# Kernel tuning notes

Measured on AMD Instinct MI355X. Metric: run time of the kernel, lower is better.

## Reference

```python
import jax, jax.numpy as jnp
import numpy as np

NUM_HEADS = 16


def setup_inputs() -> dict:
    key = jax.random.key(0)
    k1, k2, k3, k4 = jax.random.split(key, 4)
    B, N, C = 4, 1024, 1024
    x = jax.random.normal(k1, (B, N, C), dtype=jnp.float32)
    mask = jnp.ones((B, N), dtype=jnp.float32)  # 1 = visible token
    # 0.02 init scale keeps logits in a sane range (avoids saturated softmax)
    W_qkv = jax.random.normal(k2, (C, 3 * C), dtype=jnp.float32) * 0.02
    W_proj = jax.random.normal(k3, (C, C), dtype=jnp.float32) * 0.02
    b_proj = jax.random.normal(k4, (C,), dtype=jnp.float32) * 0.02
    return {"x": x, "mask": mask, "W_qkv": W_qkv, "W_proj": W_proj, "b_proj": b_proj}


def reference(x, mask, W_qkv, W_proj, b_proj):
    B, N, C = x.shape
    H = NUM_HEADS
    D = C // H
    scale = D ** -0.5
    qkv = (x @ W_qkv).reshape(B, N, 3, H, D)
    q, k, v = qkv[:, :, 0], qkv[:, :, 1], qkv[:, :, 2]  # each [B, N, H, D]
    attn = jnp.einsum("bnhd,bmhd->bhnm", q, k) * scale  # [B, H, N, N]
    attn = attn + (1.0 - mask)[:, None, None, :] * -5.0  # additive mask penalty
    attn = jax.nn.softmax(attn, axis=-1)
    out = jnp.einsum("bhnm,bmhd->bnhd", attn, v).reshape(B, N, C)
    return out @ W_proj + b_proj
```

## Files before the change

### kernel.cpp

```cpp
#include <hip/hip_runtime.h>

typedef __attribute__((ext_vector_type(8))) short bf16x8;
typedef __attribute__((ext_vector_type(4))) float f32x4;
typedef __attribute__((ext_vector_type(16))) float f32x16;
typedef __attribute__((ext_vector_type(4))) float fl4;
typedef __attribute__((ext_vector_type(8))) unsigned short u16x8;
typedef __attribute__((ext_vector_type(4))) unsigned short u16x4;
typedef __attribute__((ext_vector_type(2))) int i32x2;
typedef __attribute__((ext_vector_type(4))) int i32x4;

#define MFMA16(A,B,C) __builtin_amdgcn_mfma_f32_16x16x32_bf16((A),(B),(C),0,0,0)
#define MFMA32(A,B,C) __builtin_amdgcn_mfma_f32_32x32x16_bf16((A),(B),(C),0,0,0)

#if __has_builtin(__builtin_amdgcn_exp2f)
#define EXP2R(x) __builtin_amdgcn_exp2f(x)
#else
#define EXP2R(x) exp2f(x)
#endif

__device__ __forceinline__ unsigned short f2bf_bits(float x) {
  union { float f; unsigned u; } v; v.f = x;
  unsigned r = v.u + 0x7fffu + ((v.u >> 16) & 1u);
  return (unsigned short)(r >> 16);
}

__device__ __forceinline__ void gload_lds16(const void* g, void* l) {
  __builtin_amdgcn_global_load_lds((const __attribute__((address_space(1))) void*)g,
                                   (__attribute__((address_space(3))) void*)l, 16, 0, 0);
}

__device__ __forceinline__ int cvtpk_bf16(float a, float b) {
  int r; asm("v_cvt_pk_bf16_f32 %0, %1, %2" : "=v"(r) : "v"(a), "v"(b)); return r;
}

__device__ __forceinline__ void plswap(int& a, int& b) {
#if __has_builtin(__builtin_amdgcn_permlane32_swap)
  i32x2 r = __builtin_amdgcn_permlane32_swap(a, b, false, false);
  a = r[0]; b = r[1];
#else
  asm volatile("s_nop 1\n\tv_permlane32_swap_b32 %0, %1" : "+v"(a), "+v"(b));
#endif
}

__global__ __launch_bounds__(256) void k_prep(const float* __restrict__ x,
                                              unsigned short* __restrict__ xb,
                                              const float* __restrict__ wqkv,
                                              unsigned short* __restrict__ dqkv,
                                              const float* __restrict__ wproj,
                                              unsigned short* __restrict__ dproj) {
  __shared__ float tile[64][65];
  const int bid = blockIdx.x;
  const int t = threadIdx.x;
  if (bid < 2048) {
    int i = (bid * 256 + t) * 8;
    fl4 a = *(const fl4*)(x + i);
    fl4 b = *(const fl4*)(x + i + 4);
    u16x8 o;
    o[0] = f2bf_bits(a[0]); o[1] = f2bf_bits(a[1]); o[2] = f2bf_bits(a[2]); o[3] = f2bf_bits(a[3]);
    o[4] = f2bf_bits(b[0]); o[5] = f2bf_bits(b[1]); o[6] = f2bf_bits(b[2]); o[7] = f2bf_bits(b[3]);
    *(u16x8*)(xb + i) = o;
    return;
  }
  const int idx = bid - 2048;
  const int bx = idx & 63, by = idx >> 6;
  const float* src; unsigned short* dst; int NCOL, nt;
  if (bx < 48) { src = wqkv; dst = dqkv; NCOL = 3072; nt = bx * 64; }
  else         { src = wproj; dst = dproj; NCOL = 1024; nt = (bx - 48) * 64; }
  const float sc = (bx < 16) ? 0.18033688f : 1.0f;
  const int kt = by * 64;
  {
    int r = t >> 2, c0 = (t & 3) * 16;
    const float* s = src + (size_t)(kt + r) * NCOL + nt + c0;
    #pragma unroll
    for (int j = 0; j < 4; ++j) {
      fl4 v = *(const fl4*)(s + j * 4);
      tile[r][c0 + j * 4 + 0] = v[0]; tile[r][c0 + j * 4 + 1] = v[1];
      tile[r][c0 + j * 4 + 2] = v[2]; tile[r][c0 + j * 4 + 3] = v[3];
    }
  }
  __syncthreads();
  {
    int n = t >> 2, kc = (t & 3) * 16;
    unsigned short* d = dst + (size_t)(nt + n) * 1024 + kt + kc;
    u16x8 o0, o1;
    #pragma unroll
    for (int j = 0; j < 8; ++j) o0[j] = f2bf_bits(tile[kc + j][n] * sc);
    #pragma unroll
    for (int j = 0; j < 8; ++j) o1[j] = f2bf_bits(tile[kc + 8 + j][n] * sc);
    *(u16x8*)d = o0;
    *(u16x8*)(d + 8) = o1;
  }
}

template <int MODE>
__global__ __launch_bounds__(256) void k_gemm(const unsigned short* __restrict__ A,
                                              const unsigned short* __restrict__ Bt,
                                              unsigned short* __restrict__ qp,
                                              unsigned short* __restrict__ kp,
                                              unsigned short* __restrict__ vtp,
                                              const float* __restrict__ bias,
                                              float* __restrict__ outp) {
  __shared__ __align__(16) char lds[49152];
  const int tid = threadIdx.x, lane = tid & 63, w = tid >> 6;
  const int wm = w >> 1, wn = w & 1;
  const int m0 = blockIdx.y * 128, n0 = blockIdx.x * 128;
  const char* Ab = (const char*)A + (size_t)m0 * 2048;
  const char* Bb = (const char*)Bt + (size_t)n0 * 2048;

  int goff[2];
  #pragma unroll
  for (int i = 0; i < 2; ++i) {
    int c = i * 256 + tid;
    int lr = c >> 3, s = c & 7, p = s >> 2, kc = (s & 3) ^ (lr & 3);
    goff[i] = (((lr << 1) | p) * 2048) + (kc << 4);
  }

  int afo[4], bfo[4];
  #pragma unroll
  for (int mi = 0; mi < 4; ++mi) {
    int tr = wm * 64 + mi * 16 + (lane & 15), kc = lane >> 4;
    afo[mi] = (tr >> 1) * 128 + (tr & 1) * 64 + (((kc ^ ((tr >> 1) & 3))) << 4);
  }
  #pragma unroll
  for (int ni = 0; ni < 4; ++ni) {
    int tr = wn * 64 + ni * 16 + (lane & 15), kc = lane >> 4;
    bfo[ni] = (tr >> 1) * 128 + (tr & 1) * 64 + (((kc ^ ((tr >> 1) & 3))) << 4);
  }

  f32x4 acc[4][4];
  #pragma unroll
  for (int mi = 0; mi < 4; ++mi)
    #pragma unroll
    for (int ni = 0; ni < 4; ++ni) acc[mi][ni] = f32x4{0.f, 0.f, 0.f, 0.f};

#define GSTAGE(BUF, T)                                                         \
  do {                                                                         \
    char* dA = lds + (BUF) * 16384 + tid * 16;                                 \
    char* dB = dA + 8192;                                                      \
    gload_lds16(Ab + goff[0] + (T) * 64, dA);                                  \
    gload_lds16(Ab + goff[1] + (T) * 64, dA + 4096);                           \
    gload_lds16(Bb + goff[0] + (T) * 64, dB);                                  \
    gload_lds16(Bb + goff[1] + (T) * 64, dB + 4096);                           \
  } while (0)

#define GCOMP(BUF)                                                             \
  do {                                                                         \
    const char* LA = lds + (BUF) * 16384;                                      \
    const char* LB = LA + 8192;                                                \
    bf16x8 af[4], bfv[4];                                                      \
    _Pragma("unroll") for (int mi = 0; mi < 4; ++mi)                           \
      af[mi] = *(const bf16x8*)(LA + afo[mi]);                                 \
    _Pragma("unroll") for (int ni = 0; ni < 4; ++ni)                           \
      bfv[ni] = *(const bf16x8*)(LB + bfo[ni]);                                \
    _Pragma("unroll") for (int mi = 0; mi < 4; ++mi)                           \
      _Pragma("unroll") for (int ni = 0; ni < 4; ++ni)                         \
        acc[mi][ni] = MFMA16(af[mi], bfv[ni], acc[mi][ni]);                    \
  } while (0)

  GSTAGE(0, 0);
  GSTAGE(1, 1);
  {
    int bc = 0, bs = 2;
    for (int j = 0; j < 31; ++j) {
      asm volatile("s_waitcnt vmcnt(4)" ::: "memory");
      __builtin_amdgcn_s_barrier();
      if (j < 30) GSTAGE(bs, j + 2);
      GCOMP(bc);
      bc = (bc == 2) ? 0 : bc + 1;
      bs = (bs == 2) ? 0 : bs + 1;
    }
    asm volatile("s_waitcnt vmcnt(0)" ::: "memory");
    __builtin_amdgcn_s_barrier();
    GCOMP(1);
  }
#undef GCOMP
#undef GSTAGE

  if (MODE == 0) {
    #pragma unroll
    for (int mi = 0; mi < 4; ++mi) {
      int row0 = m0 + wm * 64 + mi * 16 + ((lane >> 4) << 2);
      int bb = row0 >> 10, nn0 = row0 & 1023;
      #pragma unroll
      for (int ni = 0; ni < 4; ++ni) {
        int col = n0 + wn * 64 + ni * 16 + (lane & 15);
        int tt = col >> 10, rem = col & 1023, h = rem >> 6, d = rem & 63;
        f32x4 a = acc[mi][ni];
        if (tt == 2) {
          u16x4 pv;
          pv[0] = f2bf_bits(a[0]); pv[1] = f2bf_bits(a[1]);
          pv[2] = f2bf_bits(a[2]); pv[3] = f2bf_bits(a[3]);
          *(u16x4*)(vtp + (((size_t)(bb * 16 + h) * 64 + d) << 10) + nn0) = pv;
        } else {
          unsigned short* dst = (tt == 0) ? qp : kp;
          size_t base = ((size_t)(bb * 16 + h)) << 16;
          #pragma unroll
          for (int r = 0; r < 4; ++r)
            dst[base + (size_t)(nn0 + r) * 64 + d] = f2bf_bits(a[r]);
        }
      }
    }
  } else {
    #pragma unroll
    for (int mi = 0; mi < 4; ++mi) {
      int row0 = m0 + wm * 64 + mi * 16 + ((lane >> 4) << 2);
      #pragma unroll
      for (int ni = 0; ni < 4; ++ni) {
        int col = n0 + wn * 64 + ni * 16 + (lane & 15);
        float bv = bias[col];
        f32x4 a = acc[mi][ni];
        #pragma unroll
        for (int r = 0; r < 4; ++r)
          outp[(size_t)(row0 + r) * 1024 + col] = a[r] + bv;
      }
    }
  }
}

__global__ __launch_bounds__(512, 4) void k_attn(const unsigned short* __restrict__ qp,
                                                 const unsigned short* __restrict__ kp,
                                                 const unsigned short* __restrict__ vtp,
                                                 const float* __restrict__ mask,
                                                 unsigned short* __restrict__ aop) {
  __shared__ __align__(16) char lds[49152];
  const int tid = threadIdx.x, lane = tid & 63, w = tid >> 6;
  const int hi = lane >> 5, lq = lane & 31;
  const int pair = w >> 2, qsub = w & 3;
  const int g = blockIdx.x;
  const int bh = (g & 7) * 8 + ((g >> 6) & 7);
  const int qc = (g >> 3) & 7;
  const int b = bh >> 4, h = bh & 15;
  const char* kb = (const char*)(kp + ((size_t)bh << 16));
  const char* vb = (const char*)(vtp + ((size_t)bh << 16));
  const unsigned short* qh = qp + ((size_t)bh << 16);
  const float* mrow = mask + b * 1024 + pair * 512;
  const int q0 = qc * 128 + qsub * 32;

  const int kpk = tid >> 8, krow = (tid >> 3) & 31, kslot = tid & 7;
  const char* gK = kb + (size_t)kpk * 65536 + (size_t)krow * 128
                   + ((kslot ^ (krow & 7)) * 16);
  const int vpk = tid >> 8, vrow = (tid >> 2) & 63, vslot = tid & 3;
  const char* gV = vb + (size_t)vpk * 1024 + (size_t)vrow * 2048
                   + ((vslot ^ ((vrow >> 1) & 3)) * 16);
  char* const dK = lds + tid * 16;
  char* const dV = lds + 8192 + tid * 16;

  int kfo[4], vfo[4];
  #pragma unroll
  for (int dc = 0; dc < 4; ++dc)
    kfo[dc] = lq * 128 + (((dc << 1) | hi) ^ (lq & 7)) * 16;
  #pragma unroll
  for (int ks = 0; ks < 2; ++ks)
    #pragma unroll
    for (int nb = 0; nb < 2; ++nb) {
      int row = nb * 32 + lq;
      vfo[ks * 2 + nb] = row * 64 + (((ks << 1) | hi) ^ ((row >> 1) & 3)) * 16;
    }

  int bws[16];
  #pragma unroll
  for (int t2 = 0; t2 < 16; ++t2) {
    float mv = mrow[t2 * 32 + lq];
    bws[t2] = (hi == 0) ? (int)f2bf_bits(fmaf(mv, 7.2134752f, -12.9842554f)) : 0;
  }

  bf16x8 qB[4];
  #pragma unroll
  for (int dc = 0; dc < 4; ++dc)
    qB[dc] = *(const bf16x8*)(qh + (q0 + lq) * 64 + dc * 16 + hi * 8);

  i32x4 onesw = {hi == 0 ? 0x3F80 : 0, 0, 0, 0};
  const bf16x8 onesB = __builtin_bit_cast(bf16x8, onesw);

  f32x16 Z16;
  #pragma unroll
  for (int i = 0; i < 16; ++i) Z16[i] = 0.f;

  f32x16 O0, O1;
  #pragma unroll
  for (int i = 0; i < 16; ++i) { O0[i] = 0.f; O1[i] = 0.f; }
  float lsum = 0.f;

#define STAGE(BUF, T)                                                          \
  do {                                                                         \
    gload_lds16(gK + (T) * 4096, dK + (BUF) * 16384);                          \
    gload_lds16(gV + (T) * 64,   dV + (BUF) * 16384);                          \
  } while (0)

#define VMCNT(N) asm volatile("s_waitcnt vmcnt(" #N ")" ::: "memory")

#define STEP(BUF, T, N)                                                        \
  do {                                                                         \
    VMCNT(N);                                                                  \
    __builtin_amdgcn_s_barrier();                                              \
    if ((T) + 2 <= 15) STAGE(((T) + 2) % 3, (T) + 2);                          \
    const char* K = lds + (BUF) * 16384 + pair * 4096;                         \
    const char* V = lds + (BUF) * 16384 + 8192 + pair * 4096;                  \
    f32x16 acc;                                                                \
    {                                                                          \
      i32x4 bwv = {bws[T], 0, 0, 0};                                           \
      acc = MFMA32(__builtin_bit_cast(bf16x8, bwv), onesB, Z16);               \
    }                                                                          \
    __builtin_amdgcn_s_setprio(1);                                             \
    _Pragma("unroll") for (int dc = 0; dc < 4; ++dc) {                         \
      bf16x8 kf = *(const bf16x8*)(K + kfo[dc]);                               \
      acc = MFMA32(kf, qB[dc], acc);                                           \
    }                                                                          \
    __builtin_amdgcn_s_setprio(0);                                             \
    float p[16];                                                               \
    _Pragma("unroll") for (int r = 0; r < 16; ++r) {                           \
      p[r] = EXP2R(acc[r]);                                                    \
      lsum += p[r];                                                            \
    }                                                                          \
    int X0 = cvtpk_bf16(p[0], p[1]),   X1 = cvtpk_bf16(p[2], p[3]);            \
    int Y0 = cvtpk_bf16(p[4], p[5]),   Y1 = cvtpk_bf16(p[6], p[7]);            \
    int Z0 = cvtpk_bf16(p[8], p[9]),   Z1 = cvtpk_bf16(p[10], p[11]);          \
    int W0 = cvtpk_bf16(p[12], p[13]), W1 = cvtpk_bf16(p[14], p[15]);          \
    plswap(X0, Y0); plswap(X1, Y1);                                            \
    plswap(Z0, W0); plswap(Z1, W1);                                            \
    i32x4 pa0v = {X0, X1, Y0, Y1};                                             \
    i32x4 pa1v = {Z0, Z1, W0, W1};                                             \
    const bf16x8 PA0 = __builtin_bit_cast(bf16x8, pa0v);                       \
    const bf16x8 PA1 = __builtin_bit_cast(bf16x8, pa1v);                       \
    bf16x8 va0 = *(const bf16x8*)(V + vfo[0]);                                 \
    bf16x8 va1 = *(const bf16x8*)(V + vfo[1]);                                 \
    bf16x8 vb0 = *(const bf16x8*)(V + vfo[2]);                                 \
    bf16x8 vb1 = *(const bf16x8*)(V + vfo[3]);                                 \
    __builtin_amdgcn_s_setprio(1);                                             \
    O0 = MFMA32(PA0, va0, O0);                                                 \
    O1 = MFMA32(PA0, va1, O1);                                                 \
    O0 = MFMA32(PA1, vb0, O0);                                                 \
    O1 = MFMA32(PA1, vb1, O1);                                                 \
    __builtin_amdgcn_s_setprio(0);                                             \
  } while (0)

  STAGE(0, 0);
  STAGE(1, 1);
  STEP(0, 0, 2);  STEP(1, 1, 2);  STEP(2, 2, 2);  STEP(0, 3, 2);
  STEP(1, 4, 2);  STEP(2, 5, 2);  STEP(0, 6, 2);  STEP(1, 7, 2);
  STEP(2, 8, 2);  STEP(0, 9, 2);  STEP(1, 10, 2); STEP(2, 11, 2);
  STEP(0, 12, 2); STEP(1, 13, 2); STEP(2, 14, 2); STEP(0, 15, 0);
#undef STEP
#undef VMCNT
#undef STAGE

  __syncthreads();
  float tot = lsum + __shfl_xor(lsum, 32);
  float* fx = (float*)lds;
  if (pair == 1) {
    int base = qsub * 64 * 34 + lane * 34;
    #pragma unroll
    for (int r = 0; r < 16; ++r) { fx[base + r] = O0[r]; fx[base + 16 + r] = O1[r]; }
    fx[base + 32] = tot;
  }
  __syncthreads();
  if (pair == 0) {
    int base = qsub * 64 * 34 + lane * 34;
    float invT = 1.0f / (tot + fx[base + 32]);
    #pragma unroll
    for (int r = 0; r < 16; ++r) {
      int qr = (r & 3) + 8 * (r >> 2) + 4 * hi;
      float iv = __shfl(invT, qr);
      float o0 = (O0[r] + fx[base + r]) * iv;
      float o1 = (O1[r] + fx[base + 16 + r]) * iv;
      size_t ob = (size_t)(b * 1024 + q0 + qr) * 1024 + h * 64 + lq;
      aop[ob] = f2bf_bits(o0);
      aop[ob + 32] = f2bf_bits(o1);
    }
  }
}

extern "C" void kernel_launch(void* const* d_in, const int* in_sizes, int n_in,
                              void* d_out, int out_size, void* d_ws, size_t ws_size,
                              hipStream_t stream) {
  const float* x     = (const float*)d_in[0];
  const float* mask  = (const float*)d_in[1];
  const float* wqkv  = (const float*)d_in[2];
  const float* wproj = (const float*)d_in[3];
  const float* bproj = (const float*)d_in[4];
  float* out = (float*)d_out;

  char* ws = (char*)d_ws;
  unsigned short* xb     = (unsigned short*)(ws);
  unsigned short* wqkvt  = (unsigned short*)(ws + 8388608);
  unsigned short* wprojt = (unsigned short*)(ws + 14680064);
  unsigned short* qbuf   = (unsigned short*)(ws + 16777216);
  unsigned short* kbuf   = (unsigned short*)(ws + 25165824);
  unsigned short* vtbuf  = (unsigned short*)(ws + 33554432);
  unsigned short* aobuf  = (unsigned short*)(ws + 41943040);

  k_prep<<<dim3(3072), dim3(256), 0, stream>>>(x, xb, wqkv, wqkvt, wproj, wprojt);
  k_gemm<0><<<dim3(24, 32), dim3(256), 0, stream>>>(xb, wqkvt, qbuf, kbuf, vtbuf, nullptr, nullptr);
  k_attn<<<dim3(512), dim3(512), 0, stream>>>(qbuf, kbuf, vtbuf, mask, aobuf);
  k_gemm<1><<<dim3(8, 32), dim3(256), 0, stream>>>(aobuf, wprojt, nullptr, nullptr, nullptr, bproj, out);
}
```

Measured before the change: 91.37 us.

## Switch GEMM to 32x32 MFMA tiles and XCD-aware block swizzle

```diff
diff --git a/kernel.cpp b/kernel.cpp
--- a/kernel.cpp
+++ b/kernel.cpp
@@ -103,7 +103,13 @@
   __shared__ __align__(16) char lds[49152];
   const int tid = threadIdx.x, lane = tid & 63, w = tid >> 6;
   const int wm = w >> 1, wn = w & 1;
-  const int m0 = blockIdx.y * 128, n0 = blockIdx.x * 128;
+  const int lq = lane & 31, hi = lane >> 5;
+  const int bid = blockIdx.x;
+  const int xcd = bid & 7, s = bid >> 3;
+  int ry, cx;
+  if (MODE == 0) { ry = (xcd & 3) * 8 + s / 12; cx = (xcd >> 2) * 12 + s % 12; }
+  else           { ry = xcd * 4 + s / 8;        cx = s % 8; }
+  const int m0 = ry * 128, n0 = cx * 128;
   const char* Ab = (const char*)A + (size_t)m0 * 2048;
   const char* Bb = (const char*)Bt + (size_t)n0 * 2048;
 
@@ -111,27 +117,28 @@
   #pragma unroll
   for (int i = 0; i < 2; ++i) {
     int c = i * 256 + tid;
-    int lr = c >> 3, s = c & 7, p = s >> 2, kc = (s & 3) ^ (lr & 3);
+    int lr = c >> 3, sl = c & 7, p = sl >> 2, kc = (sl & 3) ^ (lr & 3);
     goff[i] = (((lr << 1) | p) * 2048) + (kc << 4);
   }
 
-  int afo[4], bfo[4];
-  #pragma unroll
-  for (int mi = 0; mi < 4; ++mi) {
-    int tr = wm * 64 + mi * 16 + (lane & 15), kc = lane >> 4;
-    afo[mi] = (tr >> 1) * 128 + (tr & 1) * 64 + (((kc ^ ((tr >> 1) & 3))) << 4);
-  }
-  #pragma unroll
-  for (int ni = 0; ni < 4; ++ni) {
-    int tr = wn * 64 + ni * 16 + (lane & 15), kc = lane >> 4;
-    bfo[ni] = (tr >> 1) * 128 + (tr & 1) * 64 + (((kc ^ ((tr >> 1) & 3))) << 4);
-  }
-
-  f32x4 acc[4][4];
-  #pragma unroll
-  for (int mi = 0; mi < 4; ++mi)
-    #pragma unroll
-    for (int ni = 0; ni < 4; ++ni) acc[mi][ni] = f32x4{0.f, 0.f, 0.f, 0.f};
+  int afo[2][2], bfo[2][2];
+  #pragma unroll
+  for (int rb = 0; rb < 2; ++rb)
+    #pragma unroll
+    for (int kh = 0; kh < 2; ++kh) {
+      int tr = wm * 64 + rb * 32 + lq, ch = 2 * kh + hi;
+      afo[rb][kh] = (tr >> 1) * 128 + (tr & 1) * 64 + ((ch ^ ((tr >> 1) & 3)) << 4);
+      int tr2 = wn * 64 + rb * 32 + lq;
+      bfo[rb][kh] = (tr2 >> 1) * 128 + (tr2 & 1) * 64 + ((ch ^ ((tr2 >> 1) & 3)) << 4);
+    }
+
+  f32x16 acc2[2][2];
+  #pragma unroll
+  for (int rb = 0; rb < 2; ++rb)
+    #pragma unroll
+    for (int cb = 0; cb < 2; ++cb)
+      #pragma unroll
+      for (int i = 0; i < 16; ++i) acc2[rb][cb][i] = 0.f;
 
 #define GSTAGE(BUF, T)                                                         \
   do {                                                                         \
@@ -147,14 +154,17 @@
   do {                                                                         \
     const char* LA = lds + (BUF) * 16384;                                      \
     const char* LB = LA + 8192;                                                \
-    bf16x8 af[4], bfv[4];                                                      \
-    _Pragma("unroll") for (int mi = 0; mi < 4; ++mi)                           \
-      af[mi] = *(const bf16x8*)(LA + afo[mi]);                                 \
-    _Pragma("unroll") for (int ni = 0; ni < 4; ++ni)                           \
-      bfv[ni] = *(const bf16x8*)(LB + bfo[ni]);                                \
-    _Pragma("unroll") for (int mi = 0; mi < 4; ++mi)                           \
-      _Pragma("unroll") for (int ni = 0; ni < 4; ++ni)                         \
-        acc[mi][ni] = MFMA16(af[mi], bfv[ni], acc[mi][ni]);                    \
+    bf16x8 af[2][2], bfv[2][2];                                                \
+    _Pragma("unroll") for (int rb = 0; rb < 2; ++rb)                           \
+      _Pragma("unroll") for (int kh = 0; kh < 2; ++kh) {                       \
+        af[rb][kh]  = *(const bf16x8*)(LA + afo[rb][kh]);                      \
+        bfv[rb][kh] = *(const bf16x8*)(LB + bfo[rb][kh]);                      \
+      }                                                                        \
+    _Pragma("unroll") for (int rb = 0; rb < 2; ++rb)                           \
+      _Pragma("unroll") for (int cb = 0; cb < 2; ++cb) {                       \
+        acc2[rb][cb] = MFMA32(af[rb][0], bfv[cb][0], acc2[rb][cb]);            \
+        acc2[rb][cb] = MFMA32(af[rb][1], bfv[cb][1], acc2[rb][cb]);            \
+      }                                                                        \
   } while (0)
 
   GSTAGE(0, 0);
@@ -176,45 +186,42 @@
 #undef GCOMP
 #undef GSTAGE
 
-  if (MODE == 0) {
-    #pragma unroll
-    for (int mi = 0; mi < 4; ++mi) {
-      int row0 = m0 + wm * 64 + mi * 16 + ((lane >> 4) << 2);
-      int bb = row0 >> 10, nn0 = row0 & 1023;
-      #pragma unroll
-      for (int ni = 0; ni < 4; ++ni) {
-        int col = n0 + wn * 64 + ni * 16 + (lane & 15);
+  #pragma unroll
+  for (int rb = 0; rb < 2; ++rb)
+    #pragma unroll
+    for (int cb = 0; cb < 2; ++cb) {
+      f32x16 a = acc2[rb][cb];
+      int col = n0 + wn * 64 + cb * 32 + lq;
+      if (MODE == 0) {
         int tt = col >> 10, rem = col & 1023, h = rem >> 6, d = rem & 63;
-        f32x4 a = acc[mi][ni];
-        if (tt == 2) {
-          u16x4 pv;
-          pv[0] = f2bf_bits(a[0]); pv[1] = f2bf_bits(a[1]);
-          pv[2] = f2bf_bits(a[2]); pv[3] = f2bf_bits(a[3]);
-          *(u16x4*)(vtp + (((size_t)(bb * 16 + h) * 64 + d) << 10) + nn0) = pv;
-        } else {
-          unsigned short* dst = (tt == 0) ? qp : kp;
-          size_t base = ((size_t)(bb * 16 + h)) << 16;
+        #pragma unroll
+        for (int g4 = 0; g4 < 4; ++g4) {
+          int row0 = m0 + wm * 64 + rb * 32 + 8 * g4 + 4 * hi;
+          int bb = row0 >> 10, nn0 = row0 & 1023;
+          if (tt == 2) {
+            u16x4 pv;
+            pv[0] = f2bf_bits(a[4 * g4 + 0]); pv[1] = f2bf_bits(a[4 * g4 + 1]);
+            pv[2] = f2bf_bits(a[4 * g4 + 2]); pv[3] = f2bf_bits(a[4 * g4 + 3]);
+            *(u16x4*)(vtp + (((size_t)(bb * 16 + h) * 64 + d) << 10) + nn0) = pv;
+          } else {
+            unsigned short* dst = (tt == 0) ? qp : kp;
+            size_t base = ((size_t)(bb * 16 + h)) << 16;
+            #pragma unroll
+            for (int s2 = 0; s2 < 4; ++s2)
+              dst[base + (size_t)(nn0 + s2) * 64 + d] = f2bf_bits(a[4 * g4 + s2]);
+          }
+        }
+      } else {
+        float bv = bias[col];
+        #pragma unroll
+        for (int g4 = 0; g4 < 4; ++g4) {
+          int row0 = m0 + wm * 64 + rb * 32 + 8 * g4 + 4 * hi;
           #pragma unroll
-          for (int r = 0; r < 4; ++r)
-            dst[base + (size_t)(nn0 + r) * 64 + d] = f2bf_bits(a[r]);
+          for (int s2 = 0; s2 < 4; ++s2)
+            outp[(size_t)(row0 + s2) * 1024 + col] = a[4 * g4 + s2] + bv;
         }
       }
     }
-  } else {
-    #pragma unroll
-    for (int mi = 0; mi < 4; ++mi) {
-      int row0 = m0 + wm * 64 + mi * 16 + ((lane >> 4) << 2);
-      #pragma unroll
-      for (int ni = 0; ni < 4; ++ni) {
-        int col = n0 + wn * 64 + ni * 16 + (lane & 15);
-        float bv = bias[col];
-        f32x4 a = acc[mi][ni];
-        #pragma unroll
-        for (int r = 0; r < 4; ++r)
-          outp[(size_t)(row0 + r) * 1024 + col] = a[r] + bv;
-      }
-    }
-  }
 }
 
 __global__ __launch_bounds__(512, 4) void k_attn(const unsigned short* __restrict__ qp,
@@ -390,7 +397,7 @@
   unsigned short* aobuf  = (unsigned short*)(ws + 41943040);
 
   k_prep<<<dim3(3072), dim3(256), 0, stream>>>(x, xb, wqkv, wqkvt, wproj, wprojt);
-  k_gemm<0><<<dim3(24, 32), dim3(256), 0, stream>>>(xb, wqkvt, qbuf, kbuf, vtbuf, nullptr, nullptr);
+  k_gemm<0><<<dim3(768), dim3(256), 0, stream>>>(xb, wqkvt, qbuf, kbuf, vtbuf, nullptr, nullptr);
   k_attn<<<dim3(512), dim3(512), 0, stream>>>(qbuf, kbuf, vtbuf, mask, aobuf);
-  k_gemm<1><<<dim3(8, 32), dim3(256), 0, stream>>>(aobuf, wprojt, nullptr, nullptr, nullptr, bproj, out);
-}
+  k_gemm<1><<<dim3(256), dim3(256), 0, stream>>>(aobuf, wprojt, nullptr, nullptr, nullptr, bproj, out);
+}
```

New measurement: 89.83 us. No clear change (-1.7%).
